# Optimization experiments

Hardware: AMD Instinct MI355X
Metric: run time of the kernel (lower is better)

Reference implementation:

```python
import jax, jax.numpy as jnp
import numpy as np

N = 100000; S = 8; V = 10000; DE = 64; DH = 64; H = DH + 6; T = 2; E = 250000
MAXP = 10; SZ = 64; OUT = MAXP * SZ; NPLAIN = 6; NAR = 2


def setup_inputs() -> dict:
    key = jax.random.key(0)
    ks = jax.random.split(key, 20)
    rn = lambda k, sh, s=0.1: jax.random.normal(k, sh, jnp.float32) * s
    return {
        "tokens": jax.random.randint(ks[0], (N, S), 0, V, jnp.int32),
        "type_idx": jax.random.randint(ks[1], (N,), 0, 6, jnp.int32),
        "edge_src": jax.random.randint(ks[2], (T, E), 0, N, jnp.int32),
        "edge_dst": jax.random.randint(ks[3], (T, E), 0, N, jnp.int32),
        "map_entry_idx": 123,
        "embed": rn(ks[4], (V, DE), 0.3),
        "Wi_map": rn(ks[5], (3 * DH, DE)), "Wh_map": rn(ks[6], (3 * DH, DH)),
        "bi_map": jnp.zeros((3 * DH,), jnp.float32), "bh_map": jnp.zeros((3 * DH,), jnp.float32),
        "Wi_mem": rn(ks[7], (3 * DH, DE)), "Wh_mem": rn(ks[8], (3 * DH, DH)),
        "bi_mem": jnp.zeros((3 * DH,), jnp.float32), "bh_mem": jnp.zeros((3 * DH,), jnp.float32),
        "Wm_plain": rn(ks[9], (NPLAIN, T, H, H)), "bm_plain": jnp.zeros((NPLAIN, T, H), jnp.float32),
        "Wu_plain": rn(ks[10], (NPLAIN, 2 * H, H)), "bu_plain": jnp.zeros((NPLAIN, H), jnp.float32),
        "Wm_ar": rn(ks[11], (NAR, T, 2 * H, 2 * H)), "bm_ar": jnp.zeros((NAR, T, 2 * H), jnp.float32),
        "Wu_ar": rn(ks[12], (NAR, 4 * H, H)), "bu_ar": jnp.zeros((NAR, H), jnp.float32),
        "W1": rn(ks[13], (H, H)), "b1": jnp.zeros((H,), jnp.float32),
        "W2": rn(ks[14], (H, OUT)), "b2": jnp.zeros((OUT,), jnp.float32),
    }


def _gru_last(x_seq, Wi, Wh, bi, bh):
    # x_seq: [S, N, DE] -> last hidden [N, DH] (torch nn.GRU cell math)
    def step(h, x):
        gi = x @ Wi.T + bi
        gh = h @ Wh.T + bh
        ir, iz, inn = jnp.split(gi, 3, axis=-1)
        hr, hz, hn = jnp.split(gh, 3, axis=-1)
        r = jax.nn.sigmoid(ir + hr)
        z = jax.nn.sigmoid(iz + hz)
        n = jnp.tanh(inn + r * hn)
        return (1.0 - z) * n + z * h, None
    h0 = jnp.zeros((x_seq.shape[1], Wh.shape[1]), x_seq.dtype)
    h, _ = jax.lax.scan(step, h0, x_seq)
    return h


def _mp(h, src, dst, Wm, bm, Wu, bu, msg_act, dense_act):
    # per-edge-type linear message on sender state, scatter-max aggregation, dense update
    m = jnp.einsum('ted,tdm->tem', h[src], Wm) + bm[:, None, :]  # [T, E, M]
    if msg_act is not None:
        m = msg_act(m)
    agg = jax.ops.segment_max(m.reshape(-1, m.shape[-1]), dst.reshape(-1), num_segments=h.shape[0])
    agg = jnp.where(jnp.isneginf(agg), 0.0, agg)  # nodes with no incoming edges -> 0
    u = jnp.concatenate([h, agg], axis=-1) @ Wu + bu
    return dense_act(u) if dense_act is not None else u


def _forward(tokens, type_idx, edge_src, edge_dst, map_entry_idx, embed,
             Wi_map, Wh_map, bi_map, bh_map, Wi_mem, Wh_mem, bi_mem, bh_mem,
             Wm_plain, bm_plain, Wu_plain, bu_plain, Wm_ar, bm_ar, Wu_ar, bu_ar,
             W1, b1, W2, b2):
    x_seq = embed[tokens].transpose(1, 0, 2)  # [S, N, DE]
    h_map = _gru_last(x_seq, Wi_map, Wh_map, bi_map, bh_map)
    h_mem = _gru_last(x_seq, Wi_mem, Wh_mem, bi_mem, bh_mem)
    is_map = (type_idx == 0)[:, None]
    is_mem = (type_idx == 5)[:, None]
    node_h = jnp.where(is_map, h_map, jnp.where(is_mem, h_mem, 0.0))
    h = jnp.concatenate([jax.nn.one_hot(type_idx, 6, dtype=node_h.dtype), node_h], axis=-1)  # [N, H]
    li = 0
    for blk in range(2):  # two concat-residual blocks from create_mlp_mp_layers
        saved = h
        for _ in range(3):  # plain MLP MP layers: no msg/dense activation
            h = _mp(h, edge_src, edge_dst, Wm_plain[li], bm_plain[li], Wu_plain[li], bu_plain[li], None, None)
            li += 1
        h = jnp.concatenate([saved, h], axis=-1)  # ConcatResidualLayer -> [N, 2H]
        h = _mp(h, edge_src, edge_dst, Wm_ar[blk], bm_ar[blk], Wu_ar[blk], bu_ar[blk], jax.nn.gelu, jnp.tanh)
    x = h[map_entry_idx]            # select map entry node
    x = jax.nn.relu(x @ W1 + b1)    # trans_layers[0]
    return x @ W2 + b2


def reference(tokens, type_idx, edge_src, edge_dst, map_entry_idx, embed,
              Wi_map, Wh_map, bi_map, bh_map, Wi_mem, Wh_mem, bi_mem, bh_mem,
              Wm_plain, bm_plain, Wu_plain, bu_plain, Wm_ar, bm_ar, Wu_ar, bu_ar,
              W1, b1, W2, b2):
    return _forward(tokens, type_idx, edge_src, edge_dst, map_entry_idx, embed,
                    Wi_map, Wh_map, bi_map, bh_map, Wi_mem, Wh_mem, bi_mem, bh_mem,
                    Wm_plain, bm_plain, Wu_plain, bu_plain, Wm_ar, bm_ar, Wu_ar, bu_ar,
                    W1, b1, W2, b2)
```

## Files before the change

kernel.cpp:

```cpp
#include <hip/hip_runtime.h>
#include <math.h>

#define CAPT 20480
#define R2   (2*CAPT)
#define GLD  136
#define GRR  32

typedef __attribute__((ext_vector_type(8))) short short8;
typedef __attribute__((ext_vector_type(4))) float f32x4;

__device__ __forceinline__ float fexp2_(float x){ return __builtin_amdgcn_exp2f(x); }
__device__ __forceinline__ float frcp_(float x){ return __builtin_amdgcn_rcpf(x); }
__device__ __forceinline__ float ftanh_(float x){
  float t = fexp2_(2.885390082f * x);
  return __builtin_fmaf(-2.f, frcp_(1.f + t), 1.f);
}
__device__ __forceinline__ float fsig_(float x){
  return frcp_(1.f + fexp2_(-1.442695041f * x));
}
__device__ __forceinline__ float fgelu_(float x){
  float x2 = x*x;
  float u  = x * __builtin_fmaf(x2, 0.044715f, 1.0f);
  float e  = fexp2_(u * -2.30220818f);
  return x * frcp_(1.f + e);
}
__device__ __forceinline__ unsigned short f2bf(float x){
  unsigned int u = __float_as_uint(x);
  return (unsigned short)((u + 0x7FFFu + ((u>>16)&1u)) >> 16);
}
__device__ __forceinline__ float bf2f(unsigned short v){
  return __uint_as_float(((unsigned int)v) << 16);
}
__device__ __forceinline__ unsigned int cvt_pk_bf16(float a, float b){
  unsigned int r;
  asm("v_cvt_pk_bf16_f32 %0, %1, %2" : "=v"(r) : "v"(a), "v"(b));
  return r;
}
__device__ __forceinline__ void gload_lds16(const unsigned short* g, unsigned short* l){
  __builtin_amdgcn_global_load_lds((const __attribute__((address_space(1))) void*)g,
                                   (__attribute__((address_space(3))) void*)l, 16, 0, 0);
}

__global__ void k_prepB(const float* __restrict__ Wm_plain, const float* __restrict__ Wu_plain,
                        const float* __restrict__ Wm_ar, const float* __restrict__ Wu_ar,
                        const float* __restrict__ Wi_map, const float* __restrict__ Wh_map,
                        const float* __restrict__ Wi_mem, const float* __restrict__ Wh_mem,
                        unsigned short* __restrict__ BtArena){
  int id = blockIdx.y;
  int Kp, elems, off;
  if (id < 6){ Kp=96;  elems=15360; off=id*15360; }
  else if (id < 12){ Kp=160; elems=12800; off=92160+(id-6)*12800; }
  else if (id < 14){ Kp=160; elems=51200; off=168960+(id-12)*51200; }
  else if (id < 16){ Kp=320; elems=25600; off=271360+(id-14)*25600; }
  else { Kp=128; elems=32768; off=322560+(id-16)*32768; }
  for (int g = blockIdx.x*256 + threadIdx.x; g < elems; g += 8*256){
    int c = g / Kp, k = g - c*Kp;
    float val = 0.f;
    if (id < 6){
      int li = id; int t = (c >= 80); int cc = c - t*80;
      if (cc < 70 && k < 70) val = Wm_plain[((li*2+t)*70 + k)*70 + cc];
    } else if (id < 12){
      int li = id-6;
      int kk = (k < 70) ? k : ((k >= 80 && k < 150) ? 70 + (k-80) : -1);
      if (c < 70 && kk >= 0) val = Wu_plain[(li*140 + kk)*70 + c];
    } else if (id < 14){
      int blk = id-12; int t = (c >= 160); int cc = c - t*160;
      int kk = (k < 70) ? k : ((k >= 80 && k < 150) ? 70 + (k-80) : -1);
      if (cc < 140 && kk >= 0) val = Wm_ar[(((blk*2+t)*140) + kk)*140 + cc];
    } else if (id < 16){
      int blk = id-14;
      int kk = (k < 70) ? k : ((k >= 80 && k < 150) ? 70 + (k-80)
               : ((k >= 160 && k < 300) ? 140 + (k-160) : -1));
      if (c < 70 && kk >= 0) val = Wu_ar[(blk*280 + kk)*70 + c];
    } else {
      int typ = id-16;
      const float* Wi = typ ? Wi_mem : Wi_map;
      const float* Wh = typ ? Wh_mem : Wh_map;
      if (c < 192) val = (k < 64) ? Wi[c*64 + k] : Wh[c*64 + (k-64)];
      else { int cc = c-192; val = (k >= 64) ? Wh[(128+cc)*64 + (k-64)] : 0.f; }
    }
    BtArena[off + g] = f2bf(val);
  }
}

__global__ void k_prepBias(const float* __restrict__ bm_plain, const float* __restrict__ bu_plain,
                           const float* __restrict__ bm_ar, const float* __restrict__ bu_ar,
                           const float* __restrict__ bi_map, const float* __restrict__ bh_map,
                           const float* __restrict__ bi_mem, const float* __restrict__ bh_mem,
                           float* __restrict__ biasA){
  for (int g = threadIdx.x; g < 2752; g += 256){
    float val = 0.f;
    if (g < 960){ int li=g/160, c=g%160; int t=(c>=80); int cc=c-t*80;
      if (cc<70) val = bm_plain[(li*2+t)*70 + cc]; }
    else if (g < 1440){ int u=g-960; int li=u/80, c=u%80; if (c<70) val = bu_plain[li*70+c]; }
    else if (g < 2080){ int u=g-1440; int blk=u/320, c=u%320; int t=(c>=160); int cc=c-t*160;
      if (cc<140) val = bm_ar[(blk*2+t)*140 + cc]; }
    else if (g < 2240){ int u=g-2080; int blk=u/80, c=u%80; if (c<70) val = bu_ar[blk*70+c]; }
    else { int u=g-2240; int typ=u/256, c=u%256;
      const float* bi = typ ? bi_mem : bi_map; const float* bh = typ ? bh_mem : bh_map;
      val = (c < 192) ? (bi[c]+bh[c]) : bh[128 + (c-192)]; }
    biasA[g] = val;
  }
}

__global__ void k_prepEmb(const float* __restrict__ embed, unsigned short* __restrict__ embB,
                          int total){
  int g = blockIdx.x*256 + threadIdx.x;
  if (g < total) embB[g] = f2bf(embed[g]);
}

__global__ void k_init_h(const int* __restrict__ type_idx, unsigned short* __restrict__ h, int N){
  int g = blockIdx.x*256 + threadIdx.x;
  if (g >= N*80) return;
  int n = g / 80, c = g - n*80;
  h[g] = (c < 6 && type_idx[n] == c) ? (unsigned short)0x3F80 : (unsigned short)0;
}

__global__ void k_compact(const int* __restrict__ type_idx, int* __restrict__ idxcat,
                          int* __restrict__ cnt, int N){
  int n = blockIdx.x*256 + threadIdx.x;
  if (n >= N) return;
  int t = type_idx[n];
  if (t == 0){ int p = atomicAdd(&cnt[0],1); if (p < CAPT) idxcat[p] = n; }
  else if (t == 5){ int p = atomicAdd(&cnt[1],1); if (p < CAPT) idxcat[CAPT+p] = n; }
}

__global__ void k_count(const int* __restrict__ edst, int* __restrict__ deg, int TE){
  int i = blockIdx.x*256 + threadIdx.x;
  if (i < TE) atomicAdd(&deg[edst[i]], 1);
}
__global__ void k_scan1(const int* __restrict__ deg, int* __restrict__ off,
                        int* __restrict__ bsum, int N){
  __shared__ int sh[256];
  int t = threadIdx.x; int base = blockIdx.x*2048;
  int v[8]; int s = 0;
  for (int i=0;i<8;i++){
    int g = base + t*8 + i;
    int x = (g<N)? (((deg[g]+3)>>2)<<2) : 0;
    v[i]=x; s+=x;
  }
  sh[t]=s; __syncthreads();
  for (int o=1;o<256;o<<=1){ int x = (t>=o)? sh[t-o]:0; __syncthreads(); sh[t]+=x; __syncthreads(); }
  if (t==255) bsum[blockIdx.x] = sh[255];
  int run = sh[t]-s;
  for (int i=0;i<8;i++){ int g = base + t*8 + i; if (g<N) off[g]=run; run+=v[i]; }
}
__global__ void k_scan2(int* bsum, int nb){
  if (threadIdx.x==0 && blockIdx.x==0){
    int run=0;
    for(int b=0;b<nb;b++){ int x=bsum[b]; bsum[b]=run; run+=x; }
    bsum[nb]=run;
  }
}
__global__ void k_scan3(int* __restrict__ off, const int* __restrict__ bsum, int N, int nb){
  int g = blockIdx.x*256+threadIdx.x;
  if (g < N) off[g] += bsum[g>>11];
  if (g == 0) off[N] = bsum[nb];
}
__global__ void k_fill(const int* __restrict__ esrc, const int* __restrict__ edst,
                       const int* __restrict__ off, int* __restrict__ cur,
                       int* __restrict__ edata, int TE, int E){
  int i = blockIdx.x*256 + threadIdx.x;
  if (i >= TE) return;
  int d = edst[i];
  int pos = off[d] + atomicAdd(&cur[d], 1);
  edata[pos] = (esrc[i] << 1) | (i >= E ? 1 : 0);
}
__global__ void k_pad(const int* __restrict__ off, const int* __restrict__ cur,
                      int* __restrict__ edata, int N){
  int n = blockIdx.x*256 + threadIdx.x;
  if (n >= N) return;
  int d = cur[n];
  if (d == 0) return;
  int d4 = ((d+3)>>2)<<2;
  int base = off[n];
  int first = edata[base];
  for (int i = d; i < d4; i++) edata[base+i] = first;
}

__global__ __launch_bounds__(256) void kgru(
    const int* __restrict__ idxcat, const int* __restrict__ tokens,
    const unsigned short* __restrict__ embB,
    const unsigned short* __restrict__ Bt, const unsigned short* __restrict__ Bt2,
    const float* __restrict__ bias, const float* __restrict__ bias2,
    unsigned short* __restrict__ hOut)
{
  __shared__ __align__(16) unsigned short As[2][GRR*GLD];
  __shared__ int tokS[GRR*8];
  __shared__ int idxS[GRR];
  int rb = blockIdx.y * CAPT + blockIdx.x * GRR;
  if (idxcat[rb] < 0) return;
  int t = threadIdx.x;
  int lane = t & 63, m = lane & 15, q = lane >> 4, w = t >> 6;
  const unsigned short* Bsel = blockIdx.y ? Bt2 : Bt;
  const float* bsel = blockIdx.y ? bias2 : bias;
  short8 breg[4][4]; f32x4 bv[4];
  #pragma unroll
  for (int j=0;j<4;j++){
    int col = (w + 4*j)*16 + m;
    bv[j] = *(const f32x4*)&bsel[(w + 4*j)*16 + q*4];
    #pragma unroll
    for (int kt=0;kt<4;kt++)
      breg[j][kt] = *(const short8*)&Bsel[(size_t)col*128 + kt*32 + q*8];
  }
  if (t < GRR) idxS[t] = idxcat[rb + t];
  if (t < GRR*8){
    int nd = idxcat[rb + (t>>3)]; if (nd < 0) nd = 0;
    tokS[t] = tokens[nd*8 + (t & 7)];
  }
  __syncthreads();
  if (t < GRR*8){
    int row = t >> 3, ch = t & 7;
    *(uint4*)&As[0][row*GLD + ch*8] = *(const uint4*)&embB[(size_t)tokS[row*8]*64 + ch*8];
  }
  for (int j = t; j < GRR*32; j += 256){
    int row = j >> 5, k2 = (j & 31)*2;
    *(unsigned int*)&As[0][row*GLD + 64 + k2] = 0;
  }
  __syncthreads();
  unsigned short hreg[2][4];
  #pragma unroll
  for (int rt=0;rt<2;rt++)
    #pragma unroll
    for (int i=0;i<4;i++) hreg[rt][i] = 0;
  int u4 = w*16 + q*4;
  int p = 0;
  for (int s = 0; s < 8; s++){
    uint4 xr;
    if (s < 7 && t < GRR*8){
      int row = t >> 3, ch = t & 7;
      xr = *(const uint4*)&embB[(size_t)tokS[row*8 + s + 1]*64 + ch*8];
    }
    f32x4 acc[2][4] = {};
    #pragma unroll
    for (int kt=0;kt<4;kt++){
      short8 af[2];
      #pragma unroll
      for (int rt=0;rt<2;rt++)
        af[rt] = *(const short8*)&As[p][(rt*16+m)*GLD + kt*32 + q*8];
      #pragma unroll
      for (int j=0;j<4;j++)
        #pragma unroll
        for (int rt=0;rt<2;rt++)
          acc[rt][j] = __builtin_amdgcn_mfma_f32_16x16x32_bf16(breg[j][kt], af[rt], acc[rt][j], 0,0,0);
    }
    unsigned int plo_[2], phi_[2];
    #pragma unroll
    for (int rt=0;rt<2;rt++){
      float hv[4];
      #pragma unroll
      for (int i=0;i<4;i++){
        float xrg = acc[rt][0][i] + bv[0][i];
        float xzg = acc[rt][1][i] + bv[1][i];
        float xng = acc[rt][2][i] + bv[2][i];
        float hng = acc[rt][3][i] + bv[3][i];
        float pm = frcp_(1.f + fexp2_(1.442695041f*xrg));
        float zz = frcp_(1.f + fexp2_(-1.442695041f*xzg));
        float a  = __builtin_fmaf(-pm, hng, xng);
        float th = ftanh_(a);
        float hp = bf2f(hreg[rt][i]);
        hv[i] = __builtin_fmaf(zz, hp - th, th);
      }
      unsigned int plo = cvt_pk_bf16(hv[0], hv[1]);
      unsigned int phi = cvt_pk_bf16(hv[2], hv[3]);
      plo_[rt] = plo; phi_[rt] = phi;
      hreg[rt][0] = (unsigned short)plo;
      hreg[rt][1] = (unsigned short)(plo >> 16);
      hreg[rt][2] = (unsigned short)phi;
      hreg[rt][3] = (unsigned short)(phi >> 16);
    }
    if (s < 7){
      #pragma unroll
      for (int rt=0;rt<2;rt++){
        uint2 v; v.x = plo_[rt]; v.y = phi_[rt];
        *(uint2*)&As[p^1][(rt*16 + m)*GLD + 64 + u4] = v;
      }
      if (t < GRR*8){
        int row = t >> 3, ch = t & 7;
        *(uint4*)&As[p^1][row*GLD + ch*8] = xr;
      }
      __syncthreads();
      p ^= 1;
    } else {
      #pragma unroll
      for (int rt=0;rt<2;rt++){
        int nd = idxS[rt*16 + m];
        if (nd >= 0){
          size_t b = (size_t)nd*80 + 6 + u4;
          *(unsigned int*)&hOut[b]     = plo_[rt];
          *(unsigned int*)&hOut[b + 2] = phi_[rt];
        }
      }
    }
  }
}

template<int RTR, int KT, int CT, int ACT>
__global__ __launch_bounds__(256) void wgemm(
    const unsigned short* __restrict__ A0, int w0, int ldA0,
    const unsigned short* __restrict__ A1, int w1, int ldA1,
    const unsigned short* __restrict__ A2, int w2, int ldA2,
    const unsigned short* __restrict__ Bt, int KpB,
    const float* __restrict__ bias,
    unsigned short* __restrict__ C, int ldC,
    int rows, int tiles)
{
  constexpr int Kpad = KT*32;
  constexpr int NRT  = RTR/16;
  constexpr int NCH  = KT*4;
  constexpr int CPT  = (RTR*NCH)/256;
  __shared__ __align__(16) unsigned short As[2][RTR*Kpad];
  int t = threadIdx.x;
  int lane = t & 63, m = lane & 15, q = lane >> 4, w = t >> 6;
  int tileBase = blockIdx.y * (4*CT);
  int rtEnd = (rows + RTR - 1)/RTR;
  int tr = blockIdx.x;
  if (tr >= rtEnd) return;

  short8 breg[CT][KT]; f32x4 bv[CT]; bool val[CT]; int colb[CT];
  #pragma unroll
  for (int j=0;j<CT;j++){
    int tt = tileBase + w + 4*j;
    val[j] = (tt < tiles);
    int col = tt*16 + m;
    colb[j] = tt*16 + q*4;
    bv[j] = (f32x4){0.f,0.f,0.f,0.f};
    if (val[j]){
      bv[j] = *(const f32x4*)&bias[tt*16 + q*4];
      #pragma unroll
      for (int kt=0;kt<KT;kt++)
        breg[j][kt] = *(const short8*)&Bt[(size_t)col*KpB + kt*32 + q*8];
    } else {
      #pragma unroll
      for (int kt=0;kt<KT;kt++) breg[j][kt] = (short8){0,0,0,0,0,0,0,0};
    }
  }

  int w01 = w0 + w1, w012 = w0 + w1 + w2;

  if (w012 < NCH*8){
    const uint4 z = {0,0,0,0};
    for (int c = t; c < RTR*NCH; c += 256){
      int row = c / NCH, chp = c - row*NCH;
      if (((chp ^ (row & 3))*8) >= w012){
        *(uint4*)&As[0][c*8] = z;
        *(uint4*)&As[1][c*8] = z;
      }
    }
  }

  auto stage = [&](int p, int trr){
    #pragma unroll
    for (int i=0;i<CPT;i++){
      int c = i*256 + t;
      int row = c / NCH, chp = c - row*NCH;
      int kc = (chp ^ (row & 3))*8;
      int gr = trr*RTR + row;
      unsigned short* ldst = &As[p][(size_t)(i*256 + (t & ~63))*8];
      if (gr < rows && kc < w012){
        const unsigned short* sp;
        if (kc < w0)       sp = A0 + (size_t)gr*ldA0 + kc;
        else if (kc < w01) sp = A1 + (size_t)gr*ldA1 + (kc - w0);
        else               sp = A2 + (size_t)gr*ldA2 + (kc - w01);
        gload_lds16(sp, ldst);
      }
    }
  };

  stage(0, tr);
  __syncthreads();
  int p = 0;
  for (;;){
    int nxt = tr + gridDim.x;
    bool hasNext = (nxt < rtEnd);
    if (hasNext) stage(p^1, nxt);
    f32x4 acc[NRT][CT] = {};
    #pragma unroll
    for (int kt=0;kt<KT;kt++){
      short8 af[NRT];
      #pragma unroll
      for (int rt=0;rt<NRT;rt++)
        af[rt] = *(const short8*)&As[p][(rt*16+m)*Kpad + (((kt*4+q) ^ (m&3))*8)];
      #pragma unroll
      for (int j=0;j<CT;j++)
        #pragma unroll
        for (int rt=0;rt<NRT;rt++)
          acc[rt][j] = __builtin_amdgcn_mfma_f32_16x16x32_bf16(breg[j][kt], af[rt], acc[rt][j], 0,0,0);
    }
    bool tfull = (tr*RTR + RTR <= rows);
#define EPILOG(CHK)                                                         \
    _Pragma("unroll")                                                       \
    for (int rt=0;rt<NRT;rt++){                                             \
      int grow = tr*RTR + rt*16 + m;                                        \
      if (CHK && grow >= rows) continue;                                    \
      _Pragma("unroll")                                                     \
      for (int j=0;j<CT;j++){                                               \
        if (!val[j]) continue;                                              \
        float v0 = acc[rt][j][0] + bv[j][0];                                \
        float v1 = acc[rt][j][1] + bv[j][1];                                \
        float v2 = acc[rt][j][2] + bv[j][2];                                \
        float v3 = acc[rt][j][3] + bv[j][3];                                \
        if (ACT == 1){ v0=fgelu_(v0); v1=fgelu_(v1); v2=fgelu_(v2); v3=fgelu_(v3); } \
        else if (ACT == 2){ v0=ftanh_(v0); v1=ftanh_(v1); v2=ftanh_(v2); v3=ftanh_(v3); } \
        uint2 pk; pk.x = cvt_pk_bf16(v0, v1); pk.y = cvt_pk_bf16(v2, v3);   \
        *(uint2*)&C[(size_t)grow*ldC + colb[j]] = pk;                       \
      }                                                                     \
    }
    if (tfull){ EPILOG(false) } else { EPILOG(true) }
#undef EPILOG
    if (!hasNext) break;
    __syncthreads();
    p ^= 1; tr = nxt;
  }
}

__global__ __launch_bounds__(256) void k_aggregate(
    const int* __restrict__ off, const int* __restrict__ edata,
    const unsigned short* __restrict__ P2, int ldP, int off1,
    unsigned short* __restrict__ agg, int M, int N, int WPN)
{
  int t = threadIdx.x;
  int lane = t & 63, w = t >> 6;
  int nbase, c;
  if (WPN == 1){
    nbase = blockIdx.x*16 + w*4;
    c = 2*lane;
  } else {
    nbase = blockIdx.x*8 + (w>>1)*4;
    c = (w & 1)*80 + 2*lane;
  }
  nbase = __builtin_amdgcn_readfirstlane(nbase);
  if (nbase >= N) return;
  bool act = (lane < 40);
  const float NEG = -__builtin_inff();
  int e[4], e1[4];
  float f0[4], f1[4];
  #pragma unroll
  for (int j=0;j<4;j++){
    int n = nbase + j;
    bool v = (n < N);
    e[j]  = v ? __builtin_amdgcn_readfirstlane(off[n])     : 0;
    e1[j] = v ? __builtin_amdgcn_readfirstlane(off[n + 1]) : 0;
    f0[j] = NEG; f1[j] = NEG;
  }
  for (;;){
    bool cond[4];
    bool any = false;
    #pragma unroll
    for (int j=0;j<4;j++){ cond[j] = (e[j] < e1[j]); any |= cond[j]; }
    if (!any) break;
    unsigned int rr[4][4];
    #pragma unroll
    for (int j=0;j<4;j++){
      if (cond[j]){
        int4 g = *(const int4*)&edata[e[j]];
        int b0 = (g.x>>1)*ldP + (g.x&1)*off1;
        int b1 = (g.y>>1)*ldP + (g.y&1)*off1;
        int b2 = (g.z>>1)*ldP + (g.z&1)*off1;
        int b3 = (g.w>>1)*ldP + (g.w&1)*off1;
        if (act){
          rr[j][0] = *(const unsigned int*)(P2 + b0 + c);
          rr[j][1] = *(const unsigned int*)(P2 + b1 + c);
          rr[j][2] = *(const unsigned int*)(P2 + b2 + c);
          rr[j][3] = *(const unsigned int*)(P2 + b3 + c);
        }
      }
    }
    #pragma unroll
    for (int j=0;j<4;j++){
      if (cond[j]){
        if (act){
          unsigned int u0 = rr[j][0], u1 = rr[j][1], u2 = rr[j][2], u3 = rr[j][3];
          f0[j] = fmaxf(f0[j], fmaxf(fmaxf(__uint_as_float(u0<<16), __uint_as_float(u1<<16)),
                                     fmaxf(__uint_as_float(u2<<16), __uint_as_float(u3<<16))));
          f1[j] = fmaxf(f1[j], fmaxf(fmaxf(__uint_as_float(u0&0xFFFF0000u), __uint_as_float(u1&0xFFFF0000u)),
                                     fmaxf(__uint_as_float(u2&0xFFFF0000u), __uint_as_float(u3&0xFFFF0000u))));
        }
        e[j] += 4;
      }
    }
  }
  if (act){
    #pragma unroll
    for (int j=0;j<4;j++){
      int n = nbase + j;
      if (n >= N) continue;
      unsigned int o = (__float_as_uint(f0[j] == NEG ? 0.f : f0[j]) >> 16)
                     |  (__float_as_uint(f1[j] == NEG ? 0.f : f1[j]) & 0xFFFF0000u);
      *(unsigned int*)(agg + (size_t)n*M + c) = o;
    }
  }
}

__global__ void k_head(const unsigned short* __restrict__ h, const int* __restrict__ entry,
                       const float* __restrict__ W1, const float* __restrict__ b1,
                       const float* __restrict__ W2, const float* __restrict__ b2,
                       float* __restrict__ out){
  __shared__ float x[70], x1[70];
  int t = threadIdx.x;
  if (t < 70) x[t] = bf2f(h[(size_t)(*entry)*80 + t]);
  __syncthreads();
  if (t < 70){
    float s = b1[t];
    for (int i=0;i<70;i++) s += x[i]*W1[i*70 + t];
    x1[t] = fmaxf(s, 0.f);
  }
  __syncthreads();
  if (t < 640){
    float s = b2[t];
    for (int i=0;i<70;i++) s += x1[i]*W2[i*640 + t];
    out[t] = s;
  }
}

extern "C" void kernel_launch(void* const* d_in, const int* in_sizes, int n_in,
                              void* d_out, int out_size, void* d_ws, size_t ws_size,
                              hipStream_t stream) {
  const int*   tokens   = (const int*)d_in[0];
  const int*   type_idx = (const int*)d_in[1];
  const int*   esrc     = (const int*)d_in[2];
  const int*   edst     = (const int*)d_in[3];
  const int*   entry    = (const int*)d_in[4];
  const float* embed    = (const float*)d_in[5];
  const float* Wi_map   = (const float*)d_in[6];
  const float* Wh_map   = (const float*)d_in[7];
  const float* bi_map   = (const float*)d_in[8];
  const float* bh_map   = (const float*)d_in[9];
  const float* Wi_mem   = (const float*)d_in[10];
  const float* Wh_mem   = (const float*)d_in[11];
  const float* bi_mem   = (const float*)d_in[12];
  const float* bh_mem   = (const float*)d_in[13];
  const float* Wm_plain = (const float*)d_in[14];
  const float* bm_plain = (const float*)d_in[15];
  const float* Wu_plain = (const float*)d_in[16];
  const float* bu_plain = (const float*)d_in[17];
  const float* Wm_ar    = (const float*)d_in[18];
  const float* bm_ar    = (const float*)d_in[19];
  const float* Wu_ar    = (const float*)d_in[20];
  const float* bu_ar    = (const float*)d_in[21];
  const float* W1 = (const float*)d_in[22];
  const float* b1 = (const float*)d_in[23];
  const float* W2 = (const float*)d_in[24];
  const float* b2 = (const float*)d_in[25];
  float* out = (float*)d_out;

  const int N  = in_sizes[1];
  const int TE = in_sizes[2];
  const int E  = TE / 2;
  const int V64 = in_sizes[5];

  char* p = (char*)d_ws;
  auto alloc = [&](size_t bytes)->char* { char* r = p; p += (bytes + 255) & ~(size_t)255; return r; };
  unsigned short* hA  = (unsigned short*)alloc((size_t)N*80*2);
  unsigned short* hB  = (unsigned short*)alloc((size_t)N*80*2);
  unsigned short* hC  = (unsigned short*)alloc((size_t)N*80*2);
  unsigned short* P2  = (unsigned short*)alloc((size_t)N*320*2);
  unsigned short* agg = (unsigned short*)alloc((size_t)N*160*2);
  int* deg    = (int*)alloc((size_t)N*4);
  int* curp   = (int*)alloc((size_t)N*4);
  int* off    = (int*)alloc((size_t)(N+8)*4);
  int* edata  = (int*)alloc((size_t)(TE + 4*N + 16)*4);
  int* sbsum  = (int*)alloc(256*4);
  int* cnt    = (int*)alloc(16*4);
  int* idxcat = (int*)alloc((size_t)R2*4);
  unsigned short* BtA  = (unsigned short*)alloc(388096*2);
  float* biasA = (float*)alloc(2752*4);
  unsigned short* embB = (unsigned short*)alloc((size_t)V64*2);

  hipMemsetAsync(idxcat, 0xFF, (size_t)R2*4, stream);
  hipMemsetAsync(cnt,    0,    16*4, stream);
  hipMemsetAsync(deg,    0,    (size_t)N*4, stream);
  hipMemsetAsync(curp,   0,    (size_t)N*4, stream);

  k_prepB<<<dim3(8,18), 256, 0, stream>>>(Wm_plain, Wu_plain, Wm_ar, Wu_ar,
                                          Wi_map, Wh_map, Wi_mem, Wh_mem, BtA);
  k_prepBias<<<1, 256, 0, stream>>>(bm_plain, bu_plain, bm_ar, bu_ar,
                                    bi_map, bh_map, bi_mem, bh_mem, biasA);
  k_prepEmb<<<(V64+255)/256, 256, 0, stream>>>(embed, embB, V64);
  k_init_h<<<(N*80+255)/256, 256, 0, stream>>>(type_idx, hA, N);
  k_compact<<<(N+255)/256, 256, 0, stream>>>(type_idx, idxcat, cnt, N);

  k_count<<<(TE+255)/256, 256, 0, stream>>>(edst, deg, TE);
  int nb = (N + 2047)/2048;
  k_scan1<<<nb, 256, 0, stream>>>(deg, off, sbsum, N);
  k_scan2<<<1, 64, 0, stream>>>(sbsum, nb);
  k_scan3<<<(N+255)/256, 256, 0, stream>>>(off, sbsum, N, nb);
  k_fill<<<(TE+255)/256, 256, 0, stream>>>(esrc, edst, off, curp, edata, TE, E);
  k_pad<<<(N+255)/256, 256, 0, stream>>>(off, curp, edata, N);

  kgru<<<dim3(CAPT/GRR, 2), 256, 0, stream>>>(
      idxcat, tokens, embB,
      BtA + 322560, BtA + 322560 + 32768,
      biasA + 2240, biasA + 2240 + 256, hA);

  unsigned short* cur = hA; unsigned short* f1 = hB; unsigned short* f2 = hC;
  int li = 0;
  for (int blk = 0; blk < 2; blk++){
    unsigned short* saved = cur;
    unsigned short* ins[3]  = {cur, f1, f2};
    unsigned short* outs[3] = {f1, f2, f1};
    for (int j = 0; j < 3; j++){
      unsigned short* X = ins[j]; unsigned short* Yo = outs[j];
      wgemm<64,3,3,0><<<dim3(1024,1), 256, 0, stream>>>(
          X, 80, 80,  nullptr, 0, 0,  nullptr, 0, 0,
          BtA + li*15360, 96, biasA + li*160,
          P2, 160, N, 10);
      k_aggregate<<<(N+15)/16, 256, 0, stream>>>(off, edata, P2, 160, 80, agg, 80, N, 1);
      wgemm<64,5,2,0><<<dim3(1024,1), 256, 0, stream>>>(
          X, 80, 80,  agg, 80, 80,  nullptr, 0, 0,
          BtA + 92160 + li*12800, 160, biasA + 960 + li*80,
          Yo, 80, N, 5);
      li++;
    }
    wgemm<64,5,3,1><<<dim3(512,2), 256, 0, stream>>>(
        saved, 80, 80,  f1, 80, 80,  nullptr, 0, 0,
        BtA + 168960 + blk*51200, 160, biasA + 1440 + blk*320,
        P2, 320, N, 20);
    k_aggregate<<<(N+7)/8, 256, 0, stream>>>(off, edata, P2, 320, 160, agg, 160, N, 2);
    wgemm<32,10,2,2><<<dim3(1024,1), 256, 0, stream>>>(
        saved, 80, 80,  f1, 80, 80,  agg, 160, 160,
        BtA + 271360 + blk*25600, 320, biasA + 2080 + blk*80,
        f2, 80, N, 5);
    unsigned short* t3 = cur; cur = f2; f2 = t3;
  }

  k_head<<<1, 640, 0, stream>>>(cur, entry, W1, b1, W2, b2, out);
}
```

Baseline: 768.4 us.

## Fuse scatter-max aggregation with the dense update GEMM per 16-node tile

Replaces the separate aggregate kernel and update GEMM with one kernel. Each block gathers neighbor messages with a max reduction for 16 nodes, writes the result alongside the node's own features into swizzled shared memory, then runs MFMA for the update with bias and activation. This removes the round trip of the aggregate buffer through global memory and one launch per layer. In exchange the update GEMM now runs on small tiles with weights reloaded from global per block, and the message-passing layers 2-wide switch to 4 columns per lane.

```diff
diff --git a/kernel.cpp b/kernel.cpp
--- a/kernel.cpp
+++ b/kernel.cpp
@@ -414,42 +414,68 @@
   }
 }
 
-__global__ __launch_bounds__(256) void k_aggregate(
+template<int KT, int CPL, int ACT>
+__global__ __launch_bounds__(256) void k_aggupd(
     const int* __restrict__ off, const int* __restrict__ edata,
     const unsigned short* __restrict__ P2, int ldP, int off1,
-    unsigned short* __restrict__ agg, int M, int N, int WPN)
+    const unsigned short* __restrict__ A0,
+    const unsigned short* __restrict__ A1,
+    const unsigned short* __restrict__ Bt,
+    const float* __restrict__ bias,
+    unsigned short* __restrict__ C,
+    int N)
 {
+  constexpr int Kpad = KT*32;
+  constexpr int NCH  = KT*4;
+  constexpr int AGW  = CPL*40;
+  constexpr int KO   = Kpad - AGW;
+  constexpr int SLOTS = 16*NCH;
+  constexpr int XPT  = (SLOTS + 255)/256;
+  __shared__ __align__(16) unsigned short As[16*Kpad];
   int t = threadIdx.x;
-  int lane = t & 63, w = t >> 6;
-  int nbase, c;
-  if (WPN == 1){
-    nbase = blockIdx.x*16 + w*4;
-    c = 2*lane;
-  } else {
-    nbase = blockIdx.x*8 + (w>>1)*4;
-    c = (w & 1)*80 + 2*lane;
-  }
-  nbase = __builtin_amdgcn_readfirstlane(nbase);
-  if (nbase >= N) return;
+  int lane = t & 63, m = lane & 15, q = lane >> 4, w = t >> 6;
+  int nbase0 = blockIdx.x*16;
+  int nbase = nbase0 + w*4;
   bool act = (lane < 40);
+  int c = CPL*lane;
+
+  uint4 xreg[XPT]; bool xok[XPT];
+  #pragma unroll
+  for (int i=0;i<XPT;i++){
+    xok[i] = false;
+    int pslot = i*256 + t;
+    if (pslot < SLOTS){
+      int row = pslot / NCH, pch = pslot - row*NCH;
+      int lcol = (pch ^ (row & 3))*8;
+      int gr = nbase0 + row;
+      if (lcol < KO && gr < N){
+        const unsigned short* sp = (lcol < 80) ? (A0 + (size_t)gr*80 + lcol)
+                                               : (A1 + (size_t)gr*80 + (lcol - 80));
+        xreg[i] = *(const uint4*)sp;
+        xok[i] = true;
+      }
+    }
+  }
+
   const float NEG = -__builtin_inff();
   int e[4], e1[4];
-  float f0[4], f1[4];
+  float f[4][CPL];
   #pragma unroll
   for (int j=0;j<4;j++){
     int n = nbase + j;
     bool v = (n < N);
     e[j]  = v ? __builtin_amdgcn_readfirstlane(off[n])     : 0;
     e1[j] = v ? __builtin_amdgcn_readfirstlane(off[n + 1]) : 0;
-    f0[j] = NEG; f1[j] = NEG;
+    #pragma unroll
+    for (int i=0;i<CPL;i++) f[j][i] = NEG;
   }
   for (;;){
-    bool cond[4];
-    bool any = false;
+    bool cond[4]; bool any = false;
     #pragma unroll
     for (int j=0;j<4;j++){ cond[j] = (e[j] < e1[j]); any |= cond[j]; }
     if (!any) break;
-    unsigned int rr[4][4];
+    unsigned int   r2_[4][4];
+    uint2          r4_[4][4];
     #pragma unroll
     for (int j=0;j<4;j++){
       if (cond[j]){
@@ -459,10 +485,17 @@
         int b2 = (g.z>>1)*ldP + (g.z&1)*off1;
         int b3 = (g.w>>1)*ldP + (g.w&1)*off1;
         if (act){
-          rr[j][0] = *(const unsigned int*)(P2 + b0 + c);
-          rr[j][1] = *(const unsigned int*)(P2 + b1 + c);
-          rr[j][2] = *(const unsigned int*)(P2 + b2 + c);
-          rr[j][3] = *(const unsigned int*)(P2 + b3 + c);
+          if (CPL == 2){
+            r2_[j][0] = *(const unsigned int*)(P2 + b0 + c);
+            r2_[j][1] = *(const unsigned int*)(P2 + b1 + c);
+            r2_[j][2] = *(const unsigned int*)(P2 + b2 + c);
+            r2_[j][3] = *(const unsigned int*)(P2 + b3 + c);
+          } else {
+            r4_[j][0] = *(const uint2*)(P2 + b0 + c);
+            r4_[j][1] = *(const uint2*)(P2 + b1 + c);
+            r4_[j][2] = *(const uint2*)(P2 + b2 + c);
+            r4_[j][3] = *(const uint2*)(P2 + b3 + c);
+          }
         }
       }
     }
@@ -470,24 +503,75 @@
     for (int j=0;j<4;j++){
       if (cond[j]){
         if (act){
-          unsigned int u0 = rr[j][0], u1 = rr[j][1], u2 = rr[j][2], u3 = rr[j][3];
-          f0[j] = fmaxf(f0[j], fmaxf(fmaxf(__uint_as_float(u0<<16), __uint_as_float(u1<<16)),
-                                     fmaxf(__uint_as_float(u2<<16), __uint_as_float(u3<<16))));
-          f1[j] = fmaxf(f1[j], fmaxf(fmaxf(__uint_as_float(u0&0xFFFF0000u), __uint_as_float(u1&0xFFFF0000u)),
-                                     fmaxf(__uint_as_float(u2&0xFFFF0000u), __uint_as_float(u3&0xFFFF0000u))));
+          #pragma unroll
+          for (int k=0;k<4;k++){
+            if (CPL == 2){
+              unsigned int u = r2_[j][k];
+              f[j][0] = fmaxf(f[j][0], __uint_as_float(u << 16));
+              f[j][1] = fmaxf(f[j][1], __uint_as_float(u & 0xFFFF0000u));
+            } else {
+              uint2 u = r4_[j][k];
+              f[j][0] = fmaxf(f[j][0], __uint_as_float(u.x << 16));
+              f[j][1] = fmaxf(f[j][1], __uint_as_float(u.x & 0xFFFF0000u));
+              f[j][2] = fmaxf(f[j][2], __uint_as_float(u.y << 16));
+              f[j][3] = fmaxf(f[j][3], __uint_as_float(u.y & 0xFFFF0000u));
+            }
+          }
         }
         e[j] += 4;
       }
     }
   }
+
+  #pragma unroll
+  for (int i=0;i<XPT;i++)
+    if (xok[i]) *(uint4*)&As[(size_t)(i*256 + t)*8] = xreg[i];
   if (act){
     #pragma unroll
     for (int j=0;j<4;j++){
-      int n = nbase + j;
-      if (n >= N) continue;
-      unsigned int o = (__float_as_uint(f0[j] == NEG ? 0.f : f0[j]) >> 16)
-                     |  (__float_as_uint(f1[j] == NEG ? 0.f : f1[j]) & 0xFFFF0000u);
-      *(unsigned int*)(agg + (size_t)n*M + c) = o;
+      int row = w*4 + j;
+      int col = KO + c;
+      int lch = col >> 3, within = col & 7;
+      int phys = lch ^ (row & 3);
+      int addr = row*Kpad + phys*8 + within;
+      float g0 = (f[j][0] == NEG) ? 0.f : f[j][0];
+      float g1 = (f[j][1] == NEG) ? 0.f : f[j][1];
+      if (CPL == 2){
+        *(unsigned int*)&As[addr] = cvt_pk_bf16(g0, g1);
+      } else {
+        float g2 = (f[j][2] == NEG) ? 0.f : f[j][2];
+        float g3 = (f[j][3] == NEG) ? 0.f : f[j][3];
+        uint2 vv; vv.x = cvt_pk_bf16(g0, g1); vv.y = cvt_pk_bf16(g2, g3);
+        *(uint2*)&As[addr] = vv;
+      }
+    }
+  }
+  __syncthreads();
+
+  int nOut = nbase0 + m;
+  #pragma unroll
+  for (int jj=0;jj<2;jj++){
+    int tt = w + 4*jj;
+    if (tt < 5){
+      int col = tt*16 + m;
+      f32x4 acc = {};
+      #pragma unroll
+      for (int kt=0;kt<KT;kt++){
+        short8 bf = *(const short8*)&Bt[(size_t)col*Kpad + kt*32 + q*8];
+        short8 af = *(const short8*)&As[m*Kpad + (((kt*4+q) ^ (m&3))*8)];
+        acc = __builtin_amdgcn_mfma_f32_16x16x32_bf16(bf, af, acc, 0,0,0);
+      }
+      if (nOut < N){
+        f32x4 bvv = *(const f32x4*)&bias[tt*16 + q*4];
+        float v0 = acc[0] + bvv[0];
+        float v1 = acc[1] + bvv[1];
+        float v2 = acc[2] + bvv[2];
+        float v3 = acc[3] + bvv[3];
+        if (ACT == 1){ v0=fgelu_(v0); v1=fgelu_(v1); v2=fgelu_(v2); v3=fgelu_(v3); }
+        else if (ACT == 2){ v0=ftanh_(v0); v1=ftanh_(v1); v2=ftanh_(v2); v3=ftanh_(v3); }
+        uint2 pk; pk.x = cvt_pk_bf16(v0, v1); pk.y = cvt_pk_bf16(v2, v3);
+        *(uint2*)&C[(size_t)nOut*80 + tt*16 + q*4] = pk;
+      }
     }
   }
 }
@@ -555,7 +639,6 @@
   unsigned short* hB  = (unsigned short*)alloc((size_t)N*80*2);
   unsigned short* hC  = (unsigned short*)alloc((size_t)N*80*2);
   unsigned short* P2  = (unsigned short*)alloc((size_t)N*320*2);
-  unsigned short* agg = (unsigned short*)alloc((size_t)N*160*2);
   int* deg    = (int*)alloc((size_t)N*4);
   int* curp   = (int*)alloc((size_t)N*4);
   int* off    = (int*)alloc((size_t)(N+8)*4);
@@ -592,6 +675,8 @@
       idxcat, tokens, embB,
       BtA + 322560, BtA + 322560 + 32768,
       biasA + 2240, biasA + 2240 + 256, hA);
+
+  const int GA = (N + 15)/16;
 
   unsigned short* cur = hA; unsigned short* f1 = hB; unsigned short* f2 = hC;
   int li = 0;
@@ -605,22 +690,22 @@
           X, 80, 80,  nullptr, 0, 0,  nullptr, 0, 0,
           BtA + li*15360, 96, biasA + li*160,
           P2, 160, N, 10);
-      k_aggregate<<<(N+15)/16, 256, 0, stream>>>(off, edata, P2, 160, 80, agg, 80, N, 1);
-      wgemm<64,5,2,0><<<dim3(1024,1), 256, 0, stream>>>(
-          X, 80, 80,  agg, 80, 80,  nullptr, 0, 0,
-          BtA + 92160 + li*12800, 160, biasA + 960 + li*80,
-          Yo, 80, N, 5);
+      k_aggupd<5,2,0><<<dim3(GA,1), 256, 0, stream>>>(
+          off, edata, P2, 160, 80,
+          X, nullptr,
+          BtA + 92160 + li*12800, biasA + 960 + li*80,
+          Yo, N);
       li++;
     }
     wgemm<64,5,3,1><<<dim3(512,2), 256, 0, stream>>>(
         saved, 80, 80,  f1, 80, 80,  nullptr, 0, 0,
         BtA + 168960 + blk*51200, 160, biasA + 1440 + blk*320,
         P2, 320, N, 20);
-    k_aggregate<<<(N+7)/8, 256, 0, stream>>>(off, edata, P2, 320, 160, agg, 160, N, 2);
-    wgemm<32,10,2,2><<<dim3(1024,1), 256, 0, stream>>>(
-        saved, 80, 80,  f1, 80, 80,  agg, 160, 160,
-        BtA + 271360 + blk*25600, 320, biasA + 2080 + blk*80,
-        f2, 80, N, 5);
+    k_aggupd<10,4,2><<<dim3(GA,1), 256, 0, stream>>>(
+        off, edata, P2, 320, 160,
+        saved, f1,
+        BtA + 271360 + blk*25600, biasA + 2080 + blk*80,
+        f2, N);
     unsigned short* t3 = cur; cur = f2; f2 = t3;
   }
 
```

Measured after the change: 953.6 us. +24.1%, slower.
